# Optimization experiments

Hardware: AMD Instinct MI355X
Metric: run time of the kernel (lower is better)

## Reference

```python
import jax, jax.numpy as jnp
import numpy as np

B, C, H, W = 4, 256, 64, 64
NH, NQ, HD, WS = 4, 16, 64, 3   # num_heads, num_queries, head_dim, attn_window_size
PD = NH * HD                    # proj_dim = 256


def setup_inputs() -> dict:
    key = jax.random.key(0)
    ks = jax.random.split(key, 6)
    s = 0.02
    return {
        "x": jax.random.normal(ks[0], (B, C, H, W), jnp.float32),
        "kv_w": jax.random.normal(ks[1], (2 * PD, C), jnp.float32) * s,
        "dot_w": jax.random.normal(ks[2], (NH, NQ, HD), jnp.float32) * s,
        "head_w": jax.random.normal(ks[3], (HD, PD), jnp.float32) * s,
        "head_b": jnp.zeros((HD,), jnp.float32),
        "q_w": jax.random.normal(ks[4], (C, NQ * HD), jnp.float32) * s,
        "q_b": jnp.zeros((C,), jnp.float32),
    }


def _unfold(x, ws):
    """Sliding ws x ws patches over last two dims (stride 1, same padding).
    x: (..., h, w) -> (..., h, w, ws*ws), flattened in (i*ws + j) order
    matching torch's unfold(2).unfold(3)."""
    pad = ws // 2
    padw = [(0, 0)] * (x.ndim - 2) + [(pad, pad), (pad, pad)]
    xp = jnp.pad(x, padw)
    h, w = x.shape[-2], x.shape[-1]
    return jnp.stack(
        [xp[..., i:i + h, j:j + w] for i in range(ws) for j in range(ws)],
        axis=-1,
    )


def reference(x, kv_w, dot_w, head_w, head_b, q_w, q_b):
    b, c, h, w = x.shape
    # kv 1x1 conv, then split into k, v (each proj_dim channels)
    kv = jnp.einsum('oc,bchw->bohw', kv_w, x)
    k, v = jnp.split(kv, 2, axis=1)
    # grouped 1x1 conv: per-head head_dim -> num_queries (NOTE: no scale; the
    # original defines self.scale but never applies it in forward)
    kh = k.reshape(b, NH, HD, h, w)
    attn = jnp.einsum('bndhw,nqd->bnqhw', kh, dot_w)
    # unfold overlapping 3x3 windows (L = ws^2 = 9)
    attn_p = _unfold(attn, WS)                        # (b, n, q, h, w, L)
    v_p = _unfold(v.reshape(b, NH, HD, h, w), WS)     # (b, n, d, h, w, L)
    attn_p = jax.nn.softmax(attn_p, axis=-1)
    # per-pixel weighted sum over the window, arranged as (b, q, n, d, h, w)
    out = jnp.einsum('bnqhwl,bndhwl->bqndhw', attn_p, v_p)
    out = out.reshape(b, NQ, PD, h, w)                # (n d) -> proj_dim channels
    # head_proj: 1x1 conv proj_dim -> head_dim (dropout=0)
    y = jnp.einsum('op,bqphw->bqohw', head_w, out) + head_b[None, None, :, None, None]
    # query_proj: 1x1 conv (k*head_dim) -> dim (dropout=0)
    y = y.reshape(b, NQ * HD, h, w)
    z = jnp.einsum('oc,bchw->bohw', q_w, y) + q_b[None, :, None, None]
    return z
```

## Files before the change

kernel.cpp:

```cpp
#include <hip/hip_runtime.h>
#include <hip/hip_bf16.h>
#include <cstdint>

typedef __hip_bfloat16 bf16;
using bf16x8 = __attribute__((ext_vector_type(8))) short;
using f32x4  = __attribute__((ext_vector_type(4))) float;

#define HW_T 4096
#define B_T  4

__device__ __forceinline__ short f2bs(float f) {
    bf16 h = __float2bfloat16(f);
    return *reinterpret_cast<short*>(&h);
}
__device__ __forceinline__ float bs2f(unsigned short s) {
    unsigned int u = ((unsigned int)s) << 16;
    float f;
    __builtin_memcpy(&f, &u, 4);
    return f;
}

__global__ __launch_bounds__(256) void fuse_all(
    const float* __restrict__ kv_w, const float* __restrict__ dot_w,
    const float* __restrict__ head_w, const float* __restrict__ q_w,
    bf16* __restrict__ Wf, bf16* __restrict__ qwF)
{
    const int rb = blockIdx.x;
    if (rb < 320) {
        const int r = rb, c = threadIdx.x;
        float acc = 0.f;
        int rowIdx;
        if (r < 64) {
            const int n = r >> 4, q = r & 15;
            #pragma unroll 8
            for (int d = 0; d < 64; ++d)
                acc += dot_w[(n * 16 + q) * 64 + d] * kv_w[(size_t)(n * 64 + d) * 256 + c];
            rowIdx = r;
        } else {
            const int rr = r - 64, n = rr >> 6, dh = rr & 63;
            #pragma unroll 8
            for (int dd = 0; dd < 64; ++dd)
                acc += head_w[dh * 256 + n * 64 + dd] * kv_w[(size_t)(256 + n * 64 + dd) * 256 + c];
            rowIdx = 64 + dh * 4 + n;
        }
        Wf[((size_t)(c >> 3) * 320 + rowIdx) * 8 + (c & 7)] = __float2bfloat16(acc);
    } else {
        const int t  = (rb - 320) * 256 + threadIdx.x;
        const int ch = t & 255, kb = t >> 8;
        const float* src = q_w + (size_t)ch * 1024 + kb * 8;
        bf16x8 pk;
        #pragma unroll
        for (int j = 0; j < 8; ++j) pk[j] = f2bs(src[j]);
        *(bf16x8*)&qwF[(size_t)t * 8] = pk;
    }
}

__global__ __launch_bounds__(256) void gemm_xw(
    const float* __restrict__ x, const bf16* __restrict__ Wf,
    bf16* __restrict__ AH)
{
    __shared__ __align__(16) bf16 As[2][8][32][8];
    const int tid  = threadIdx.x;
    const int lane = tid & 63;
    const int wave = tid >> 6;
    const int p0 = blockIdx.x * 32;
    const int b  = blockIdx.y;
    const float* xb = x + (size_t)b * 256 * HW_T;
    const int fi = lane & 15, quad = lane >> 4;
    const int wn0 = wave * 80;

    const int spx = tid & 31, sc8 = tid >> 5;

    f32x4 acc[2][5] = {};
    float xr[8];
    bf16x8 bcur[2][5], bnxt[2][5];

    {
        const float* xp = xb + (size_t)(sc8 * 8) * HW_T + p0 + spx;
        #pragma unroll
        for (int j = 0; j < 8; ++j) xr[j] = xp[(size_t)j * HW_T];
        #pragma unroll
        for (int c = 0; c < 2; ++c)
            #pragma unroll
            for (int j = 0; j < 5; ++j)
                bcur[c][j] = *(const bf16x8*)
                    &Wf[((size_t)(c * 4 + quad) * 320 + wn0 + j * 16 + fi) * 8];
        bf16x8 pk;
        #pragma unroll
        for (int j = 0; j < 8; ++j) pk[j] = f2bs(xr[j]);
        *(bf16x8*)&As[0][sc8][spx][0] = pk;
    }

    #pragma unroll
    for (int it = 0; it < 4; ++it) {
        const int cur = it & 1;
        __syncthreads();
        if (it < 3) {
            const int k1 = (it + 1) * 64;
            const float* xp = xb + (size_t)(k1 + sc8 * 8) * HW_T + p0 + spx;
            #pragma unroll
            for (int j = 0; j < 8; ++j) xr[j] = xp[(size_t)j * HW_T];
            #pragma unroll
            for (int c = 0; c < 2; ++c)
                #pragma unroll
                for (int j = 0; j < 5; ++j)
                    bnxt[c][j] = *(const bf16x8*)
                        &Wf[((size_t)((k1 >> 3) + c * 4 + quad) * 320 + wn0 + j * 16 + fi) * 8];
        }
        #pragma unroll
        for (int c = 0; c < 2; ++c) {
            bf16x8 af[2];
            #pragma unroll
            for (int i = 0; i < 2; ++i)
                af[i] = *(const bf16x8*)&As[cur][c * 4 + quad][i * 16 + fi][0];
            #pragma unroll
            for (int i = 0; i < 2; ++i)
                #pragma unroll
                for (int j = 0; j < 5; ++j)
                    acc[i][j] = __builtin_amdgcn_mfma_f32_16x16x32_bf16(
                        af[i], bcur[c][j], acc[i][j], 0, 0, 0);
        }
        if (it < 3) {
            bf16x8 pk;
            #pragma unroll
            for (int j = 0; j < 8; ++j) pk[j] = f2bs(xr[j]);
            *(bf16x8*)&As[cur ^ 1][sc8][spx][0] = pk;
            #pragma unroll
            for (int c = 0; c < 2; ++c)
                #pragma unroll
                for (int j = 0; j < 5; ++j) bcur[c][j] = bnxt[c][j];
        }
    }

    bf16* Cp = AH + ((size_t)b * HW_T + p0) * 320;
    #pragma unroll
    for (int i = 0; i < 2; ++i) {
        const int pl = i * 16 + quad * 4;
        #pragma unroll
        for (int r = 0; r < 4; ++r)
            #pragma unroll
            for (int j = 0; j < 5; ++j)
                Cp[(size_t)(pl + r) * 320 + wn0 + j * 16 + fi] =
                    __float2bfloat16(acc[i][j][r]);
    }
}

#define YPAD 1032
#define ATTN_LDS (32 * YPAD * 2 + 4 * 9 * 64 * 4)

__global__ __launch_bounds__(256) void attn_qy(
    const bf16* __restrict__ AH, const float* __restrict__ head_b,
    const bf16* __restrict__ qwF, const float* __restrict__ q_b,
    float* __restrict__ z)
{
    extern __shared__ __align__(16) char smem[];
    bf16*  yL = (bf16*)smem;
    float* Pm = (float*)(smem + 32 * YPAD * 2) + (threadIdx.x >> 6) * 9 * 64;

    const int tid  = threadIdx.x;
    const int wave = tid >> 6, lane = tid & 63;
    const int half = blockIdx.x & 1;
    const int h    = (blockIdx.x >> 1) & 63;
    const int b    = blockIdx.x >> 7;
    const int w0   = half * 32;
    const int hw0  = h * 64 + w0;
    const int fi = lane & 15, quad = lane >> 4;
    const ushort* AHu = (const ushort*)AH;

    float hb[4];
    #pragma unroll
    for (int dt = 0; dt < 4; ++dt) hb[dt] = head_b[dt * 16 + fi];

    for (int pi = 0; pi < 8; ++pi) {
        const int lp = wave * 8 + pi;
        const int w  = w0 + lp;
        int off[9]; float okf[9];
        #pragma unroll
        for (int l = 0; l < 9; ++l) {
            const int i = l / 3, j = l % 3;
            const int hh = h + i - 1, ww = w + j - 1;
            const bool ok = ((unsigned)hh < 64u) && ((unsigned)ww < 64u);
            off[l] = ((b << 12) + (ok ? hh : h) * 64 + (ok ? ww : w)) * 320;
            okf[l] = ok ? 1.0f : 0.0f;
        }
        {
            float lg[9];
            #pragma unroll
            for (int l = 0; l < 9; ++l)
                lg[l] = bs2f(AHu[(size_t)off[l] + lane]) * okf[l];
            float m = lg[0];
            #pragma unroll
            for (int l = 1; l < 9; ++l) m = fmaxf(m, lg[l]);
            float e[9], s = 0.f;
            #pragma unroll
            for (int l = 0; l < 9; ++l) { e[l] = __expf(lg[l] - m); s += e[l]; }
            const float inv = 1.0f / s;
            #pragma unroll
            for (int l = 0; l < 9; ++l) Pm[l * 64 + lane] = e[l] * inv * okf[l];
        }

        bf16x8 afr;
        #pragma unroll
        for (int j = 0; j < 8; ++j) {
            const int k = quad * 8 + j;
            afr[j] = f2bs(Pm[(k >> 2) * 64 + (k & 3) * 16 + fi]);
        }
        f32x4 acc[4];
        #pragma unroll
        for (int dt = 0; dt < 4; ++dt) {
            acc[dt][0] = hb[dt]; acc[dt][1] = hb[dt];
            acc[dt][2] = hb[dt]; acc[dt][3] = hb[dt];
        }
        #pragma unroll
        for (int dt = 0; dt < 4; ++dt) {
            const int d = dt * 16 + fi;
            const ushort4 u0 = *(const ushort4*)&AHu[(size_t)off[quad * 2]     + 64 + d * 4];
            const ushort4 u1 = *(const ushort4*)&AHu[(size_t)off[quad * 2 + 1] + 64 + d * 4];
            bf16x8 bfr;
            bfr[0] = (short)u0.x; bfr[1] = (short)u0.y;
            bfr[2] = (short)u0.z; bfr[3] = (short)u0.w;
            bfr[4] = (short)u1.x; bfr[5] = (short)u1.y;
            bfr[6] = (short)u1.z; bfr[7] = (short)u1.w;
            acc[dt] = __builtin_amdgcn_mfma_f32_16x16x32_bf16(afr, bfr, acc[dt], 0, 0, 0);
        }
        {
            float pv[4][4];
            #pragma unroll
            for (int n = 0; n < 4; ++n)
                #pragma unroll
                for (int r = 0; r < 4; ++r)
                    pv[n][r] = Pm[8 * 64 + n * 16 + quad * 4 + r];
            #pragma unroll
            for (int dt = 0; dt < 4; ++dt) {
                const int d = dt * 16 + fi;
                const ushort4 u = *(const ushort4*)&AHu[(size_t)off[8] + 64 + d * 4];
                const float h0 = bs2f(u.x), h1 = bs2f(u.y), h2 = bs2f(u.z), h3 = bs2f(u.w);
                #pragma unroll
                for (int r = 0; r < 4; ++r) {
                    float a = acc[dt][r];
                    a = fmaf(pv[0][r], h0, a);
                    a = fmaf(pv[1][r], h1, a);
                    a = fmaf(pv[2][r], h2, a);
                    a = fmaf(pv[3][r], h3, a);
                    acc[dt][r] = a;
                }
            }
        }
        #pragma unroll
        for (int dt = 0; dt < 4; ++dt)
            #pragma unroll
            for (int r = 0; r < 4; ++r)
                yL[(size_t)lp * YPAD + (quad * 4 + r) * 64 + dt * 16 + fi] =
                    __float2bfloat16(acc[dt][r]);
    }
    __syncthreads();

    f32x4 zacc[4][2] = {};
    bf16x8 af[4], afn[4];
    #pragma unroll
    for (int i = 0; i < 4; ++i)
        af[i] = *(const bf16x8*)&qwF[((size_t)quad * 256 + wave * 64 + i * 16 + fi) * 8];

    #pragma unroll 2
    for (int k0 = 0; k0 < 1024; k0 += 32) {
        if (k0 < 992) {
            const size_t kb = (size_t)((k0 + 32) >> 3) + quad;
            #pragma unroll
            for (int i = 0; i < 4; ++i)
                afn[i] = *(const bf16x8*)&qwF[(kb * 256 + wave * 64 + i * 16 + fi) * 8];
        }
        bf16x8 bfr[2];
        #pragma unroll
        for (int j = 0; j < 2; ++j)
            bfr[j] = *(const bf16x8*)&yL[(size_t)(j * 16 + fi) * YPAD + k0 + quad * 8];
        #pragma unroll
        for (int i = 0; i < 4; ++i)
            #pragma unroll
            for (int j = 0; j < 2; ++j)
                zacc[i][j] = __builtin_amdgcn_mfma_f32_16x16x32_bf16(
                    af[i], bfr[j], zacc[i][j], 0, 0, 0);
        #pragma unroll
        for (int i = 0; i < 4; ++i) af[i] = afn[i];
    }

    #pragma unroll
    for (int i = 0; i < 4; ++i) {
        const int row0 = wave * 64 + i * 16 + quad * 4;
        #pragma unroll
        for (int r = 0; r < 4; ++r) {
            const float bv = q_b[row0 + r];
            #pragma unroll
            for (int j = 0; j < 2; ++j)
                z[((size_t)(b * 256 + row0 + r)) * HW_T + hw0 + j * 16 + fi] =
                    zacc[i][j][r] + bv;
        }
    }
}

extern "C" void kernel_launch(void* const* d_in, const int* in_sizes, int n_in,
                              void* d_out, int out_size, void* d_ws, size_t ws_size,
                              hipStream_t stream) {
    (void)in_sizes; (void)n_in; (void)out_size; (void)ws_size;
    const float* x      = (const float*)d_in[0];
    const float* kv_w   = (const float*)d_in[1];
    const float* dot_w  = (const float*)d_in[2];
    const float* head_w = (const float*)d_in[3];
    const float* head_b = (const float*)d_in[4];
    const float* q_w    = (const float*)d_in[5];
    const float* q_b    = (const float*)d_in[6];
    float* z = (float*)d_out;

    char* ws   = (char*)d_ws;
    bf16*  AH  = (bf16*)ws;
    bf16*  qwF = (bf16*)(ws + 10485760);
    bf16*  Wf  = (bf16*)(ws + 11010048);

    static bool attr_done = []() {
        hipFuncSetAttribute((const void*)attn_qy,
                            hipFuncAttributeMaxDynamicSharedMemorySize, ATTN_LDS);
        return true;
    }();
    (void)attr_done;

    fuse_all<<<dim3(448), 256, 0, stream>>>(kv_w, dot_w, head_w, q_w, Wf, qwF);

    gemm_xw<<<dim3(128, B_T), 256, 0, stream>>>(x, Wf, AH);

    attn_qy<<<dim3(512), 256, ATTN_LDS, stream>>>(AH, head_b, qwF, q_b, z);
}
```

Baseline: 113.9 us.

## Widen attn_qy tiles to full rows, MFMA the ninth tap, swizzle LDS

The attention+query-projection kernel now processes a full 64-pixel row per block with 512 threads (8 waves) instead of half rows with 256 threads. This halves the number of blocks and lets each wave reuse each q_w fragment across 4 pixel tiles instead of 2. The ninth window tap is computed with an extra zero-padded MFMA instead of scalar FMAs, and the softmax probabilities are stored in LDS as bf16 with a padded stride. An XOR swizzle on the y buffer is meant to reduce LDS bank conflicts. In exchange, LDS use per block roughly doubles and there are only 256 blocks, which lowers occupancy and leaves the 256 CUs with fewer blocks to balance.

```diff
diff --git a/kernel.cpp b/kernel.cpp
--- a/kernel.cpp
+++ b/kernel.cpp
@@ -146,24 +146,26 @@
 }
 
 #define YPAD 1032
-#define ATTN_LDS (32 * YPAD * 2 + 4 * 9 * 64 * 4)
-
-__global__ __launch_bounds__(256) void attn_qy(
+#define PSTR 72
+#define ATTN_LDS (64 * YPAD * 2 + 8 * 9 * PSTR * 2)
+
+__device__ __forceinline__ int ysw(int ch) {
+    return ch ^ (((ch >> 8) & 3) << 4);
+}
+
+__global__ __launch_bounds__(512) void attn_qy(
     const bf16* __restrict__ AH, const float* __restrict__ head_b,
     const bf16* __restrict__ qwF, const float* __restrict__ q_b,
     float* __restrict__ z)
 {
     extern __shared__ __align__(16) char smem[];
-    bf16*  yL = (bf16*)smem;
-    float* Pm = (float*)(smem + 32 * YPAD * 2) + (threadIdx.x >> 6) * 9 * 64;
+    bf16*  yL  = (bf16*)smem;
+    short* Pmb = (short*)(smem + 64 * YPAD * 2) + (threadIdx.x >> 6) * 9 * PSTR;
 
     const int tid  = threadIdx.x;
     const int wave = tid >> 6, lane = tid & 63;
-    const int half = blockIdx.x & 1;
-    const int h    = (blockIdx.x >> 1) & 63;
-    const int b    = blockIdx.x >> 7;
-    const int w0   = half * 32;
-    const int hw0  = h * 64 + w0;
+    const int h    = blockIdx.x & 63;
+    const int b    = blockIdx.x >> 6;
     const int fi = lane & 15, quad = lane >> 4;
     const ushort* AHu = (const ushort*)AH;
 
@@ -173,7 +175,7 @@
 
     for (int pi = 0; pi < 8; ++pi) {
         const int lp = wave * 8 + pi;
-        const int w  = w0 + lp;
+        const int w  = lp;
         int off[9]; float okf[9];
         #pragma unroll
         for (int l = 0; l < 9; ++l) {
@@ -196,15 +198,23 @@
             for (int l = 0; l < 9; ++l) { e[l] = __expf(lg[l] - m); s += e[l]; }
             const float inv = 1.0f / s;
             #pragma unroll
-            for (int l = 0; l < 9; ++l) Pm[l * 64 + lane] = e[l] * inv * okf[l];
+            for (int l = 0; l < 9; ++l)
+                Pmb[l * PSTR + lane] = f2bs(e[l] * inv * okf[l]);
         }
 
         bf16x8 afr;
         #pragma unroll
         for (int j = 0; j < 8; ++j) {
             const int k = quad * 8 + j;
-            afr[j] = f2bs(Pm[(k >> 2) * 64 + (k & 3) * 16 + fi]);
-        }
+            afr[j] = Pmb[(k >> 2) * PSTR + (k & 3) * 16 + fi];
+        }
+        bf16x8 afr2;
+        #pragma unroll
+        for (int j = 0; j < 8; ++j) afr2[j] = 0;
+        #pragma unroll
+        for (int j = 0; j < 4; ++j)
+            afr2[j] = (quad == 0) ? Pmb[8 * PSTR + j * 16 + fi] : (short)0;
+
         f32x4 acc[4];
         #pragma unroll
         for (int dt = 0; dt < 4; ++dt) {
@@ -222,75 +232,66 @@
             bfr[4] = (short)u1.x; bfr[5] = (short)u1.y;
             bfr[6] = (short)u1.z; bfr[7] = (short)u1.w;
             acc[dt] = __builtin_amdgcn_mfma_f32_16x16x32_bf16(afr, bfr, acc[dt], 0, 0, 0);
-        }
-        {
-            float pv[4][4];
-            #pragma unroll
-            for (int n = 0; n < 4; ++n)
-                #pragma unroll
-                for (int r = 0; r < 4; ++r)
-                    pv[n][r] = Pm[8 * 64 + n * 16 + quad * 4 + r];
-            #pragma unroll
-            for (int dt = 0; dt < 4; ++dt) {
-                const int d = dt * 16 + fi;
-                const ushort4 u = *(const ushort4*)&AHu[(size_t)off[8] + 64 + d * 4];
-                const float h0 = bs2f(u.x), h1 = bs2f(u.y), h2 = bs2f(u.z), h3 = bs2f(u.w);
-                #pragma unroll
-                for (int r = 0; r < 4; ++r) {
-                    float a = acc[dt][r];
-                    a = fmaf(pv[0][r], h0, a);
-                    a = fmaf(pv[1][r], h1, a);
-                    a = fmaf(pv[2][r], h2, a);
-                    a = fmaf(pv[3][r], h3, a);
-                    acc[dt][r] = a;
-                }
+            const ushort4 u8v = *(const ushort4*)&AHu[(size_t)off[8] + 64 + d * 4];
+            bf16x8 bfr2;
+            #pragma unroll
+            for (int j = 0; j < 8; ++j) bfr2[j] = 0;
+            if (quad == 0) {
+                bfr2[0] = (short)u8v.x; bfr2[1] = (short)u8v.y;
+                bfr2[2] = (short)u8v.z; bfr2[3] = (short)u8v.w;
             }
+            acc[dt] = __builtin_amdgcn_mfma_f32_16x16x32_bf16(afr2, bfr2, acc[dt], 0, 0, 0);
         }
         #pragma unroll
         for (int dt = 0; dt < 4; ++dt)
             #pragma unroll
-            for (int r = 0; r < 4; ++r)
-                yL[(size_t)lp * YPAD + (quad * 4 + r) * 64 + dt * 16 + fi] =
-                    __float2bfloat16(acc[dt][r]);
+            for (int r = 0; r < 4; ++r) {
+                const int ch = quad * 256 + r * 64 + dt * 16 + fi;
+                yL[(size_t)lp * YPAD + ysw(ch)] = __float2bfloat16(acc[dt][r]);
+            }
     }
     __syncthreads();
 
-    f32x4 zacc[4][2] = {};
-    bf16x8 af[4], afn[4];
-    #pragma unroll
-    for (int i = 0; i < 4; ++i)
-        af[i] = *(const bf16x8*)&qwF[((size_t)quad * 256 + wave * 64 + i * 16 + fi) * 8];
+    f32x4 zacc[2][4] = {};
+    bf16x8 af[2], afn[2];
+    #pragma unroll
+    for (int i = 0; i < 2; ++i)
+        af[i] = *(const bf16x8*)&qwF[((size_t)quad * 256 + wave * 32 + i * 16 + fi) * 8];
 
     #pragma unroll 2
     for (int k0 = 0; k0 < 1024; k0 += 32) {
         if (k0 < 992) {
             const size_t kb = (size_t)((k0 + 32) >> 3) + quad;
             #pragma unroll
-            for (int i = 0; i < 4; ++i)
-                afn[i] = *(const bf16x8*)&qwF[(kb * 256 + wave * 64 + i * 16 + fi) * 8];
-        }
-        bf16x8 bfr[2];
-        #pragma unroll
-        for (int j = 0; j < 2; ++j)
-            bfr[j] = *(const bf16x8*)&yL[(size_t)(j * 16 + fi) * YPAD + k0 + quad * 8];
-        #pragma unroll
-        for (int i = 0; i < 4; ++i)
-            #pragma unroll
-            for (int j = 0; j < 2; ++j)
+            for (int i = 0; i < 2; ++i)
+                afn[i] = *(const bf16x8*)&qwF[(kb * 256 + wave * 32 + i * 16 + fi) * 8];
+        }
+        const int chs = ysw(k0 + quad * 8);
+        bf16x8 bfr[4];
+        #pragma unroll
+        for (int j = 0; j < 4; ++j)
+            bfr[j] = *(const bf16x8*)&yL[(size_t)(j * 16 + fi) * YPAD + chs];
+        #pragma unroll
+        for (int i = 0; i < 2; ++i)
+            #pragma unroll
+            for (int j = 0; j < 4; ++j)
                 zacc[i][j] = __builtin_amdgcn_mfma_f32_16x16x32_bf16(
                     af[i], bfr[j], zacc[i][j], 0, 0, 0);
-        #pragma unroll
-        for (int i = 0; i < 4; ++i) af[i] = afn[i];
-    }
-
-    #pragma unroll
-    for (int i = 0; i < 4; ++i) {
-        const int row0 = wave * 64 + i * 16 + quad * 4;
+        if (k0 < 992) {
+            #pragma unroll
+            for (int i = 0; i < 2; ++i) af[i] = afn[i];
+        }
+    }
+
+    const int hw0 = h * 64;
+    #pragma unroll
+    for (int i = 0; i < 2; ++i) {
+        const int row0 = wave * 32 + i * 16 + quad * 4;
         #pragma unroll
         for (int r = 0; r < 4; ++r) {
             const float bv = q_b[row0 + r];
             #pragma unroll
-            for (int j = 0; j < 2; ++j)
+            for (int j = 0; j < 4; ++j)
                 z[((size_t)(b * 256 + row0 + r)) * HW_T + hw0 + j * 16 + fi] =
                     zacc[i][j][r] + bv;
         }
@@ -326,5 +327,5 @@
 
     gemm_xw<<<dim3(128, B_T), 256, 0, stream>>>(x, Wf, AH);
 
-    attn_qy<<<dim3(512), 256, ATTN_LDS, stream>>>(AH, head_b, qwF, q_b, z);
-}
+    attn_qy<<<dim3(256), 512, ATTN_LDS, stream>>>(AH, head_b, qwF, q_b, z);
+}
```

After: 114.3 us. No clear change (+0.3%).
